# Performance work log

Measured on AMD Instinct MI355X. Metric: run time of the kernel, lower is better.

Reference implementation:

```python
import jax, jax.numpy as jnp
import numpy as np

N = 4096
NODE_DIM = 256
HIDDEN = 64
N_CLASSES = 16
N_HEADS = 4
NEG_SLOPE = 0.01  # F.leaky_relu default


def _xavier(key, shape):
    fan_out, fan_in = shape[0], shape[1]
    limit = float(np.sqrt(6.0 / (fan_in + fan_out)))
    return jax.random.uniform(key, shape, jnp.float32, -limit, limit)


def setup_inputs() -> dict:
    key = jax.random.key(0)
    ks = jax.random.split(key, 8)
    x = jax.random.normal(ks[0], (N, NODE_DIM), jnp.float32)
    adj_mat = jax.random.randint(ks[1], (N, N), 0, 2, jnp.int32)
    # head-stacked layer-1 params
    W1 = _xavier(ks[2], (N_HEADS * HIDDEN, NODE_DIM)).reshape(N_HEADS, HIDDEN, NODE_DIM)
    a1_1 = _xavier(ks[3], (N_HEADS * HIDDEN, 1)).reshape(N_HEADS, HIDDEN)
    a2_1 = _xavier(ks[4], (N_HEADS * HIDDEN, 1)).reshape(N_HEADS, HIDDEN)
    # layer-2 params
    W2 = _xavier(ks[5], (N_CLASSES, N_HEADS * HIDDEN))
    a1_2 = _xavier(ks[6], (N_CLASSES, 1))[:, 0]
    a2_2 = _xavier(ks[7], (N_CLASSES, 1))[:, 0]
    return {"x": x, "adj_mat": adj_mat, "W1": W1, "a1_1": a1_1, "a2_1": a2_1,
            "W2": W2, "a1_2": a1_2, "a2_2": a2_2}


def _attention_layer(x, adj_f, W, a1, a2):
    # x: [N, in_dim], W: [out_dim, in_dim], a1/a2: [out_dim]
    h = x @ W.T                               # [N, d]
    f1 = h @ a1                               # [N]
    f2 = h @ a2                               # [N]
    e = jax.nn.leaky_relu(f1[:, None] + f2[None, :], NEG_SLOPE)  # [N, N]
    e = e * adj_f
    e = jnp.where(e == 0, -jnp.inf, e)        # faithful to torch.where(e==0, -inf, e)
    alpha = jax.nn.softmax(e, axis=1)         # [N, N]
    return alpha @ h                          # [N, d]


def reference(x, adj_mat, W1, a1_1, a2_1, W2, a1_2, a2_2):
    adj_f = adj_mat.astype(x.dtype)
    # layer 1: vmap over heads, concat along feature dim
    heads = jax.vmap(_attention_layer, in_axes=(None, None, 0, 0, 0))(
        x, adj_f, W1, a1_1, a2_1)              # [H, N, hidden]
    h = jnp.transpose(heads, (1, 0, 2)).reshape(N, N_HEADS * HIDDEN)
    h = jax.nn.elu(h)
    # dropout p=0.0 -> identity
    logits = _attention_layer(h, adj_f, W2, a1_2, a2_2)  # [N, n_classes]
    return logits
```

## Files before the change

### kernel.cpp

```cpp
#include <hip/hip_runtime.h>
#include <cstdint>

typedef __bf16 bf16x8 __attribute__((ext_vector_type(8)));
typedef float  f32x4  __attribute__((ext_vector_type(4)));

#define LOG2E 1.4426950408889634f

__device__ __forceinline__ void split8(const float* v, bf16x8& hi, bf16x8& lo) {
    union { bf16x8 v; __bf16 e[8]; } h, l;
    #pragma unroll
    for (int j = 0; j < 8; j++) {
        __bf16 hb = (__bf16)v[j];
        float  r  = v[j] - (float)hb;
        h.e[j] = hb; l.e[j] = (__bf16)r;
    }
    hi = h.v; lo = l.v;
}
__device__ __forceinline__ bf16x8 cvt8(const float* v) {
    union { bf16x8 v; __bf16 e[8]; } u;
    #pragma unroll
    for (int j = 0; j < 8; j++) u.e[j] = (__bf16)v[j];
    return u.v;
}
__device__ __forceinline__ void splitstore(unsigned short* ph, unsigned short* pl, float v) {
    __bf16 hb = (__bf16)v;
    float  r  = v - (float)hb;
    __bf16 lb = (__bf16)r;
    unsigned short hu, lu;
    __builtin_memcpy(&hu, &hb, 2); __builtin_memcpy(&lu, &lb, 2);
    *ph = hu; *pl = lu;
}
__device__ __forceinline__ unsigned short f2bfh(float v) {
    __bf16 hb = (__bf16)v; unsigned short hu;
    __builtin_memcpy(&hu, &hb, 2); return hu;
}

__global__ __launch_bounds__(256)
void kzero(float4* __restrict__ p) {
    p[blockIdx.x * 256 + threadIdx.x] = float4{0.f, 0.f, 0.f, 0.f};
}

__global__ __launch_bounds__(256)
void kpre(const int* __restrict__ adj, unsigned long long* __restrict__ bm64,
          const float* __restrict__ w1, const float* __restrict__ w2,
          unsigned short* __restrict__ w1h, unsigned short* __restrict__ w1l,
          unsigned short* __restrict__ w2h, unsigned short* __restrict__ w2l) {
    int bx = blockIdx.x, tid = threadIdx.x;
    if (bx < 8192) {
        int row = bx >> 1, jbase = (bx & 1) * 2048;
        int wave = tid >> 6, lane = tid & 63;
        const int* base = adj + (size_t)row * 4096 + jbase + wave * 512;
        unsigned long long* bmw = bm64 + row * 64 + (jbase >> 6) + wave * 8;
        #pragma unroll
        for (int it = 0; it < 8; it++) {
            int v = base[it * 64 + lane];
            unsigned long long mask = __ballot(v != 0);
            if (lane == 0) bmw[it] = mask;
        }
        return;
    }
    int e = ((bx - 8192) * 256 + tid) * 4;
    const float* src; unsigned short *dh, *dl;
    if (e < 65536) { src = w1 + e; dh = w1h + e; dl = w1l + e; }
    else { int e2 = e - 65536; src = w2 + e2; dh = w2h + e2; dl = w2l + e2; }
    #pragma unroll
    for (int j = 0; j < 4; j++) splitstore(dh + j, dl + j, src[j]);
}

__global__ __launch_bounds__(256)
void k1_gemm(const float* __restrict__ x,
             const unsigned short* __restrict__ w1h,
             const unsigned short* __restrict__ w1l,
             const float* __restrict__ a11, const float* __restrict__ a21,
             unsigned short* __restrict__ h1t_hi, float* __restrict__ fvals) {
    int tid = threadIdx.x, wave = tid >> 6, lane = tid & 63;
    int q = lane >> 4, m = lane & 15;
    int i0 = blockIdx.x * 16;
    int c0 = wave * 64;
    f32x4 acc[4] = {};
    #pragma unroll
    for (int k0 = 0; k0 < 256; k0 += 32) {
        bf16x8 ah, al;
        split8(x + (i0 + m) * 256 + k0 + q * 8, ah, al);
        #pragma unroll
        for (int ct = 0; ct < 4; ct++) {
            bf16x8 bh = *(const bf16x8*)(w1h + (c0 + ct * 16 + m) * 256 + k0 + q * 8);
            bf16x8 bl = *(const bf16x8*)(w1l + (c0 + ct * 16 + m) * 256 + k0 + q * 8);
            acc[ct] = __builtin_amdgcn_mfma_f32_16x16x32_bf16(ah, bh, acc[ct], 0, 0, 0);
            acc[ct] = __builtin_amdgcn_mfma_f32_16x16x32_bf16(al, bh, acc[ct], 0, 0, 0);
            acc[ct] = __builtin_amdgcn_mfma_f32_16x16x32_bf16(ah, bl, acc[ct], 0, 0, 0);
        }
    }
    float a1v[4], a2v[4];
    #pragma unroll
    for (int ct = 0; ct < 4; ct++) {
        a1v[ct] = a11[wave * 64 + ct * 16 + m];
        a2v[ct] = a21[wave * 64 + ct * 16 + m];
    }
    #pragma unroll
    for (int r = 0; r < 4; r++) {
        int i = i0 + q * 4 + r;
        float s1 = 0.f, s2 = 0.f;
        #pragma unroll
        for (int ct = 0; ct < 4; ct++) {
            int c = c0 + ct * 16 + m;
            h1t_hi[c * 4096 + i] = f2bfh(acc[ct][r]);
            s1 += acc[ct][r] * a1v[ct];
            s2 += acc[ct][r] * a2v[ct];
        }
        #pragma unroll
        for (int off = 1; off < 16; off <<= 1) {
            s1 += __shfl_xor(s1, off);
            s2 += __shfl_xor(s2, off);
        }
        if (m == 0) {
            fvals[wave * 4096 + i] = s1 * LOG2E;
            fvals[16384 + wave * 4096 + i] = s2 * LOG2E;
        }
    }
}

template<int NCT, int JLEN, bool ATOM>
__global__ __launch_bounds__(256)
void attn_kernel(const unsigned char* __restrict__ bmb,
                 const float* __restrict__ f1_all,
                 const float* __restrict__ f2_all,
                 const unsigned short* __restrict__ BTh_all,
                 float* __restrict__ pacc,
                 float* __restrict__ zacc,
                 int pstride) {
    constexpr int S    = JLEN / 32;
    constexpr int ST   = (S % 8 == 0) ? S + 4 : S;
    constexpr int PR   = S / 4;
    constexpr int R    = 64;
    constexpr int NU4  = R * PR;
    constexpr int CR   = NCT * 16;
    constexpr int TSTR = 40;
    int tid = threadIdx.x, wave = tid >> 6, lane = tid & 63;
    int q = lane >> 4, m = lane & 15;
    int head = blockIdx.y;
    int i0 = blockIdx.x * R;
    int jstart = blockIdx.z * JLEN;

    if (!ATOM) {
        pacc += (size_t)blockIdx.z * (size_t)(4096 * pstride);
        zacc += (size_t)blockIdx.z * (size_t)((NCT == 4 ? 4 : 1) * 4096);
    }

    __shared__ unsigned int ldsbm[R * ST];
    __shared__ unsigned short ldsbt[2][CR * TSTR];
    __shared__ float ldsf2[JLEN];

    const unsigned short* BTh = BTh_all + (size_t)head * CR * 4096;
    const float* f1 = f1_all + head * 4096;
    const float* f2 = f2_all + head * 4096;

    for (int c = tid; c < NU4; c += 256) {
        int row = c / PR, part = c % PR;
        uint4 v = *(const uint4*)(bmb + (size_t)(i0 + row) * 512 + (jstart >> 3) + part * 16);
        *(uint4*)&ldsbm[row * ST + part * 4] = v;
    }
    for (int c = tid; c < JLEN / 4; c += 256)
        *(float4*)&ldsf2[c * 4] = *(const float4*)(f2 + jstart + c * 4);
    uint4 vstage;
    int sc = tid >> 2, sp = tid & 3;
    if (tid < CR * 4) {
        vstage = *(const uint4*)(BTh + (size_t)sc * 4096 + jstart + sp * 8);
        *(uint4*)&ldsbt[0][sc * TSTR + sp * 8] = vstage;
    }

    int col0 = head * CR;
    int r0 = wave * 16;
    float f1s0 = f1[i0 + r0 + m];

    f32x4 acc0[NCT] = {};
    float z0 = 0.f;

    constexpr int NIT = JLEN / 32;
    for (int it = 0; it < NIT; it++) {
        __syncthreads();
        int jl = it * 32;
        if (it + 1 < NIT && tid < CR * 4)
            vstage = *(const uint4*)(BTh + (size_t)sc * 4096 + jstart + jl + 32 + sp * 8);

        unsigned int md0 = ldsbm[(r0 + m) * ST + (jl >> 5)];
        const float4* f2p = (const float4*)&ldsf2[jl + q * 8];
        float4 fa = f2p[0], fb = f2p[1];
        float fv[8] = {fa.x, fa.y, fa.z, fa.w, fb.x, fb.y, fb.z, fb.w};
        float pv0[8];
        #pragma unroll
        for (int jj = 0; jj < 8; jj++) {
            int bit = q * 8 + jj;
            float s0 = f1s0 + fv[jj];
            float e0 = fmaxf(s0, 0.01f * s0);
            bool v0 = ((md0 >> bit) & 1u) && (s0 != 0.0f);
            float p0 = v0 ? __builtin_amdgcn_exp2f(e0) : 0.0f;
            z0 += p0; pv0[jj] = p0;
        }
        bf16x8 ah0 = cvt8(pv0);
        int cur = it & 1;
        #pragma unroll
        for (int ct = 0; ct < NCT; ct++) {
            bf16x8 bh = *(const bf16x8*)&ldsbt[cur][(ct * 16 + m) * TSTR + q * 8];
            acc0[ct] = __builtin_amdgcn_mfma_f32_16x16x32_bf16(ah0, bh, acc0[ct], 0, 0, 0);
        }
        if (it + 1 < NIT && tid < CR * 4)
            *(uint4*)&ldsbt[1 - cur][sc * TSTR + sp * 8] = vstage;
    }
    z0 += __shfl_xor(z0, 16); z0 += __shfl_xor(z0, 32);
    if (lane < 16) {
        if (ATOM) {
            atomicAdd(&zacc[head * 4096 + i0 + r0 + lane], z0);
        } else {
            zacc[head * 4096 + i0 + r0 + lane] = z0;
        }
    }
    #pragma unroll
    for (int ct = 0; ct < NCT; ct++)
        #pragma unroll
        for (int r = 0; r < 4; r++) {
            int col = col0 + ct * 16 + m;
            int rowA = i0 + r0 + q * 4 + r;
            if (ATOM) {
                atomicAdd(&pacc[rowA * pstride + col], acc0[ct][r]);
            } else {
                pacc[rowA * pstride + col] = acc0[ct][r];
            }
        }
}

__global__ __launch_bounds__(256)
void fin1c(const float* __restrict__ pp, const float* __restrict__ zp, int nj,
           unsigned short* __restrict__ hh, unsigned short* __restrict__ hl) {
    int row = blockIdx.x, col = threadIdx.x;
    float s = 0.f;
    for (int jc = 0; jc < nj; jc++) s += pp[(size_t)jc * (4096 * 256) + row * 256 + col];
    int head = col >> 6;
    float zz = 0.f;
    for (int jc = 0; jc < nj; jc++) zz += zp[jc * (4 * 4096) + head * 4096 + row];
    float v = s / zz;
    v = (v > 0.f) ? v : (__expf(v) - 1.0f);
    splitstore(&hh[row * 256 + col], &hl[row * 256 + col], v);
}

__global__ __launch_bounds__(256)
void k3_layer2(const unsigned short* __restrict__ helu_hi,
               const unsigned short* __restrict__ helu_lo,
               const unsigned short* __restrict__ w2h,
               const unsigned short* __restrict__ w2l,
               const float* __restrict__ a12,
               const float* __restrict__ a22,
               unsigned short* __restrict__ h2t_hi,
               float* __restrict__ fq) {
    int tid = threadIdx.x, wave = tid >> 6, lane = tid & 63;
    int q = lane >> 4, m = lane & 15;
    int i0 = (blockIdx.x * 4 + wave) * 16;
    f32x4 acc = {};
    #pragma unroll
    for (int k0 = 0; k0 < 256; k0 += 32) {
        bf16x8 ah = *(const bf16x8*)(helu_hi + (i0 + m) * 256 + k0 + q * 8);
        bf16x8 al = *(const bf16x8*)(helu_lo + (i0 + m) * 256 + k0 + q * 8);
        bf16x8 bh = *(const bf16x8*)(w2h + m * 256 + k0 + q * 8);
        bf16x8 bl = *(const bf16x8*)(w2l + m * 256 + k0 + q * 8);
        acc = __builtin_amdgcn_mfma_f32_16x16x32_bf16(ah, bh, acc, 0, 0, 0);
        acc = __builtin_amdgcn_mfma_f32_16x16x32_bf16(al, bh, acc, 0, 0, 0);
        acc = __builtin_amdgcn_mfma_f32_16x16x32_bf16(ah, bl, acc, 0, 0, 0);
    }
    float a1v = a12[m], a2v = a22[m];
    #pragma unroll
    for (int r = 0; r < 4; r++) {
        float v = acc[r];
        int i = i0 + q * 4 + r;
        h2t_hi[m * 4096 + i] = f2bfh(v);
        float s1 = v * a1v, s2 = v * a2v;
        #pragma unroll
        for (int off = 1; off < 16; off <<= 1) {
            s1 += __shfl_xor(s1, off);
            s2 += __shfl_xor(s2, off);
        }
        if (m == 0) { fq[i] = s1 * LOG2E; fq[4096 + i] = s2 * LOG2E; }
    }
}

__global__ __launch_bounds__(256)
void fin2(const float* __restrict__ pp, const float* __restrict__ zp, int nj,
          float* __restrict__ out) {
    int idx = blockIdx.x * 256 + threadIdx.x;
    float s = 0.f;
    for (int jc = 0; jc < nj; jc++) s += pp[jc * 65536 + idx];
    float zz = 0.f;
    for (int jc = 0; jc < nj; jc++) zz += zp[jc * 4096 + (idx >> 4)];
    out[idx] = s / zz;
}

extern "C" void kernel_launch(void* const* d_in, const int* in_sizes, int n_in,
                              void* d_out, int out_size, void* d_ws, size_t ws_size,
                              hipStream_t stream) {
    const float* x   = (const float*)d_in[0];
    const int*   adj = (const int*)d_in[1];
    const float* w1  = (const float*)d_in[2];
    const float* a11 = (const float*)d_in[3];
    const float* a21 = (const float*)d_in[4];
    const float* w2  = (const float*)d_in[5];
    const float* a12 = (const float*)d_in[6];
    const float* a22 = (const float*)d_in[7];
    float* out = (float*)d_out;

    uint8_t* w = (uint8_t*)d_ws;
    unsigned long long* bm  = (unsigned long long*)(w);
    unsigned short* h1t_hi  = (unsigned short*)(w + (2u << 20));
    unsigned short* h2t_hi  = (unsigned short*)(w + (4u << 20));
    float*          fvals   = (float*)(w + (4u << 20) + (128u << 10));
    float*          fq      = (float*)(w + (4u << 20) + (256u << 10));
    unsigned short* w1h     = (unsigned short*)(w + (4u << 20) + (288u << 10));
    unsigned short* w1l     = (unsigned short*)(w + (4u << 20) + (416u << 10));
    unsigned short* w2h     = (unsigned short*)(w + (4u << 20) + (544u << 10));
    unsigned short* w2l     = (unsigned short*)(w + (4u << 20) + (552u << 10));
    unsigned short* helu_hi = (unsigned short*)(w + (4u << 20) + (560u << 10));
    unsigned short* helu_lo = (unsigned short*)(w + (4u << 20) + (2608u << 10));

    bool big = ws_size >= ((size_t)48 << 20);
    float* p1 = (float*)(w + (9u << 20));
    float *z1, *p2, *z2;
    if (big) {
        z1 = p1 + (size_t)4 * 4096 * 256;
        p2 = z1 + 4 * 4 * 4096;
        z2 = p2 + (size_t)16 * 4096 * 16;
    } else {
        z1 = p1 + 4096 * 256;
        p2 = z1 + 4 * 4096;
        z2 = p2 + 4096 * 16;
    }

    if (!big) kzero<<<1108, 256, 0, stream>>>((float4*)p1);
    kpre<<<8260, 256, 0, stream>>>(adj, bm, w1, w2, w1h, w1l, w2h, w2l);
    k1_gemm<<<256, 256, 0, stream>>>(x, w1h, w1l, a11, a21, h1t_hi, fvals);
    if (big)
        attn_kernel<4, 1024, false><<<dim3(64, 4, 4), 256, 0, stream>>>(
            (const unsigned char*)bm, fvals, fvals + 16384, h1t_hi, p1, z1, 256);
    else
        attn_kernel<4, 1024, true><<<dim3(64, 4, 4), 256, 0, stream>>>(
            (const unsigned char*)bm, fvals, fvals + 16384, h1t_hi, p1, z1, 256);
    fin1c<<<4096, 256, 0, stream>>>(p1, z1, big ? 4 : 1, helu_hi, helu_lo);
    k3_layer2<<<64, 256, 0, stream>>>(helu_hi, helu_lo, w2h, w2l, a12, a22,
                                      h2t_hi, fq);
    if (big)
        attn_kernel<1, 256, false><<<dim3(64, 1, 16), 256, 0, stream>>>(
            (const unsigned char*)bm, fq, fq + 4096, h2t_hi, p2, z2, 16);
    else
        attn_kernel<1, 256, true><<<dim3(64, 1, 16), 256, 0, stream>>>(
            (const unsigned char*)bm, fq, fq + 4096, h2t_hi, p2, z2, 16);
    fin2<<<256, 256, 0, stream>>>(p2, z2, big ? 16 : 1, out);
}
```

Measured before the change: 189.7 us.

## Load B operand fragments directly from global into registers, drop LDS staging

Removes the double-buffered LDS staging of the per-head value matrix and its per-iteration __syncthreads. Each wave now loads its own MFMA B fragments straight from global memory into registers, prefetching the next 32-column step one iteration ahead. This drops barrier and LDS traffic from the main loop. In exchange, all four waves redundantly fetch the same B data through L1/L2 with strided 16-byte loads, and register pressure rises.

```diff
diff --git a/kernel.cpp b/kernel.cpp
--- a/kernel.cpp
+++ b/kernel.cpp
@@ -135,7 +135,6 @@
     constexpr int R    = 64;
     constexpr int NU4  = R * PR;
     constexpr int CR   = NCT * 16;
-    constexpr int TSTR = 40;
     int tid = threadIdx.x, wave = tid >> 6, lane = tid & 63;
     int q = lane >> 4, m = lane & 15;
     int head = blockIdx.y;
@@ -148,7 +147,6 @@
     }
 
     __shared__ unsigned int ldsbm[R * ST];
-    __shared__ unsigned short ldsbt[2][CR * TSTR];
     __shared__ float ldsf2[JLEN];
 
     const unsigned short* BTh = BTh_all + (size_t)head * CR * 4096;
@@ -162,12 +160,7 @@
     }
     for (int c = tid; c < JLEN / 4; c += 256)
         *(float4*)&ldsf2[c * 4] = *(const float4*)(f2 + jstart + c * 4);
-    uint4 vstage;
-    int sc = tid >> 2, sp = tid & 3;
-    if (tid < CR * 4) {
-        vstage = *(const uint4*)(BTh + (size_t)sc * 4096 + jstart + sp * 8);
-        *(uint4*)&ldsbt[0][sc * TSTR + sp * 8] = vstage;
-    }
+    __syncthreads();
 
     int col0 = head * CR;
     int r0 = wave * 16;
@@ -176,13 +169,21 @@
     f32x4 acc0[NCT] = {};
     float z0 = 0.f;
 
+    const unsigned short* bbase = BTh + (size_t)m * 4096 + jstart + q * 8;
+
+    bf16x8 bcur[NCT], bnxt[NCT];
+    #pragma unroll
+    for (int ct = 0; ct < NCT; ct++)
+        bcur[ct] = *(const bf16x8*)(bbase + (size_t)ct * 16 * 4096);
+
     constexpr int NIT = JLEN / 32;
     for (int it = 0; it < NIT; it++) {
-        __syncthreads();
         int jl = it * 32;
-        if (it + 1 < NIT && tid < CR * 4)
-            vstage = *(const uint4*)(BTh + (size_t)sc * 4096 + jstart + jl + 32 + sp * 8);
-
+        if (it + 1 < NIT) {
+            #pragma unroll
+            for (int ct = 0; ct < NCT; ct++)
+                bnxt[ct] = *(const bf16x8*)(bbase + (size_t)ct * 16 * 4096 + jl + 32);
+        }
         unsigned int md0 = ldsbm[(r0 + m) * ST + (jl >> 5)];
         const float4* f2p = (const float4*)&ldsf2[jl + q * 8];
         float4 fa = f2p[0], fb = f2p[1];
@@ -198,14 +199,12 @@
             z0 += p0; pv0[jj] = p0;
         }
         bf16x8 ah0 = cvt8(pv0);
-        int cur = it & 1;
-        #pragma unroll
-        for (int ct = 0; ct < NCT; ct++) {
-            bf16x8 bh = *(const bf16x8*)&ldsbt[cur][(ct * 16 + m) * TSTR + q * 8];
-            acc0[ct] = __builtin_amdgcn_mfma_f32_16x16x32_bf16(ah0, bh, acc0[ct], 0, 0, 0);
-        }
-        if (it + 1 < NIT && tid < CR * 4)
-            *(uint4*)&ldsbt[1 - cur][sc * TSTR + sp * 8] = vstage;
+        #pragma unroll
+        for (int ct = 0; ct < NCT; ct++)
+            acc0[ct] = __builtin_amdgcn_mfma_f32_16x16x32_bf16(ah0, bcur[ct], acc0[ct], 0, 0, 0);
+        #pragma unroll
+        for (int ct = 0; ct < NCT; ct++)
+            bcur[ct] = bnxt[ct];
     }
     z0 += __shfl_xor(z0, 16); z0 += __shfl_xor(z0, 32);
     if (lane < 16) {
```

Result: slower. 222.1 us (+17.1%).
